# Optimization experiments

Hardware: AMD Instinct MI355X
Metric: run time of the kernel (lower is better)

Reference implementation:

```python
import jax, jax.numpy as jnp
import numpy as np

D_MODEL = 2048
NHEADS = 16
HEAD_DIM = D_MODEL // NHEADS


def setup_inputs() -> dict:
    key = jax.random.key(0)
    kx, kq, kk, kv, ko = jax.random.split(key, 5)
    B, S = 2, 2048
    scale = 1.0 / np.sqrt(D_MODEL)
    return {
        "x": jax.random.normal(kx, (B, S, D_MODEL), dtype=jnp.float32),
        "Wq": jax.random.normal(kq, (D_MODEL, D_MODEL), dtype=jnp.float32) * scale,
        "Wk": jax.random.normal(kk, (D_MODEL, D_MODEL), dtype=jnp.float32) * scale,
        "Wv": jax.random.normal(kv, (D_MODEL, D_MODEL), dtype=jnp.float32) * scale,
        "Wo": jax.random.normal(ko, (D_MODEL, D_MODEL), dtype=jnp.float32) * scale,
    }


def reference(x, Wq, Wk, Wv, Wo):
    B, S, _ = x.shape
    # nn.Linear(bias=False): y = x @ W.T
    q = (x @ Wq.T).reshape(B, S, NHEADS, HEAD_DIM)
    k = (x @ Wk.T).reshape(B, S, NHEADS, HEAD_DIM)
    v = (x @ Wv.T).reshape(B, S, NHEADS, HEAD_DIM)
    sm_scale = 1.0 / np.sqrt(HEAD_DIM)
    # scores: [B, H, S, S]
    scores = jnp.einsum("bqhd,bkhd->bhqk", q, k) * sm_scale
    causal_mask = jnp.tril(jnp.ones((S, S), dtype=bool))  # [S, S]
    scores = jnp.where(causal_mask, scores, jnp.finfo(scores.dtype).min)
    probs = jax.nn.softmax(scores, axis=-1)
    attn = jnp.einsum("bhqk,bkhd->bqhd", probs, v)  # [B, S, H, D]
    out = attn.reshape(B, S, D_MODEL) @ Wo.T
    return out
```

## Files before the change

kernel.cpp:

```cpp
#include <hip/hip_runtime.h>
#include <hip/hip_bf16.h>
#include <type_traits>

#define DEV __device__ __forceinline__

typedef __bf16 bf16x8 __attribute__((ext_vector_type(8)));
typedef float f32x4 __attribute__((ext_vector_type(4)));
typedef float f32x16 __attribute__((ext_vector_type(16)));
typedef unsigned short u16;
typedef unsigned int u32;

DEV u16 f32_to_bf16(float f) {
  union { float f; u32 u; } x; x.f = f;
  u32 r = (x.u + 0x7FFFu + ((x.u >> 16) & 1u)) >> 16;
  return (u16)r;
}

DEV u32 pack2(float a, float b) {
  union { __hip_bfloat162 h; u32 u; } c;
  c.h = __float22bfloat162_rn(float2{a, b});
  return c.u;
}

DEV void ld_lds16(const void* g, void* l) {
  __builtin_amdgcn_global_load_lds(
      (const __attribute__((address_space(1))) u32*)g,
      (__attribute__((address_space(3))) u32*)l, 16, 0, 0);
}

#define MFMA16(a, b, c) __builtin_amdgcn_mfma_f32_16x16x32_bf16(a, b, c, 0, 0, 0)
#define MFMA32(a, b, c) __builtin_amdgcn_mfma_f32_32x32x16_bf16(a, b, c, 0, 0, 0)

__global__ __launch_bounds__(256) void cast_all(
    const float* __restrict__ x,  const float* __restrict__ wq,
    const float* __restrict__ wk, const float* __restrict__ wv,
    const float* __restrict__ wo,
    u16* __restrict__ xb,  u16* __restrict__ wqb, u16* __restrict__ wkb,
    u16* __restrict__ wvb, u16* __restrict__ wob) {
  int bid = blockIdx.x;
  const float* src; u16* dst; int base;
  if (bid < 8192)       { src = x;  dst = xb;  base = bid; }
  else if (bid < 12288) { src = wq; dst = wqb; base = bid - 8192; }
  else if (bid < 16384) { src = wk; dst = wkb; base = bid - 12288; }
  else if (bid < 20480) { src = wv; dst = wvb; base = bid - 16384; }
  else                  { src = wo; dst = wob; base = bid - 20480; }
  int i = (base * 256 + threadIdx.x) * 4;
  float4 v = *reinterpret_cast<const float4*>(src + i);
  ushort4 o;
  o.x = f32_to_bf16(v.x); o.y = f32_to_bf16(v.y);
  o.z = f32_to_bf16(v.z); o.w = f32_to_bf16(v.w);
  *reinterpret_cast<ushort4*>(dst + i) = o;
}

template <typename OutT>
__global__ __launch_bounds__(256) void gemm_nt(const u16* __restrict__ A,
                                               const u16* __restrict__ B,
                                               OutT* __restrict__ C,
                                               int M, int N, int K,
                                               float oscLo, float oscHi, int nsplit) {
  __shared__ __align__(16) u16 sA[128 * 64];
  __shared__ __align__(16) u16 sB[128 * 64];
  const int tid = threadIdx.x;
  const int lane = tid & 63, wid = tid >> 6;
  const int lo = lane & 15, hi = lane >> 4;
  const int wm = wid >> 1, wn = wid & 1;
  const int m0 = blockIdx.y * 128, n0 = blockIdx.x * 128;
  const float osc = (n0 < nsplit) ? oscLo : oscHi;

  f32x4 acc[4][4] = {};

  for (int k0 = 0; k0 < K; k0 += 64) {
    __syncthreads();
#pragma unroll
    for (int i = 0; i < 4; ++i) {
      int e16 = i * 256 + tid;
      int r = e16 >> 3;
      int bcol = ((e16 & 7) * 16) ^ ((r & 7) << 4);
      int col = bcol >> 1;
      ld_lds16(A + (size_t)(m0 + r) * K + k0 + col, sA + e16 * 8);
      ld_lds16(B + (size_t)(n0 + r) * K + k0 + col, sB + e16 * 8);
    }
    __syncthreads();
#pragma unroll
    for (int kc = 0; kc < 2; ++kc) {
      bf16x8 a[4], b[4];
#pragma unroll
      for (int i = 0; i < 4; ++i) {
        int row = wm * 64 + i * 16 + lo;
        int boff = ((kc * 32 + hi * 8) * 2) ^ ((row & 7) << 4);
        a[i] = *(const bf16x8*)((const char*)sA + row * 128 + boff);
      }
#pragma unroll
      for (int i = 0; i < 4; ++i) {
        int row = wn * 64 + i * 16 + lo;
        int boff = ((kc * 32 + hi * 8) * 2) ^ ((row & 7) << 4);
        b[i] = *(const bf16x8*)((const char*)sB + row * 128 + boff);
      }
#pragma unroll
      for (int mi = 0; mi < 4; ++mi)
#pragma unroll
        for (int ni = 0; ni < 4; ++ni)
          acc[mi][ni] = MFMA16(a[mi], b[ni], acc[mi][ni]);
    }
  }
#pragma unroll
  for (int mi = 0; mi < 4; ++mi)
#pragma unroll
    for (int r = 0; r < 4; ++r) {
      size_t row = m0 + wm * 64 + mi * 16 + hi * 4 + r;
#pragma unroll
      for (int ni = 0; ni < 4; ++ni) {
        int col = n0 + wn * 64 + ni * 16 + lo;
        float v = acc[mi][ni][r] * osc;
        if constexpr (std::is_same<OutT, float>::value)
          C[row * N + col] = v;
        else
          C[row * N + col] = f32_to_bf16(v);
      }
    }
}

constexpr float RTHR2 = 11.5416f;

__global__ __launch_bounds__(256, 2) void attn_fwd(const u16* __restrict__ QK,
                                                   const u16* __restrict__ VT,
                                                   u16* __restrict__ O) {
  __shared__ __align__(16) u16 sK[2][64 * 128];

  const int x = blockIdx.x, h = blockIdx.y, b = blockIdx.z;
  const int qt = b ? x : (15 - x);
  const int tid = threadIdx.x;
  const int lane = tid & 63, wid = tid >> 6;
  const int l31 = lane & 31, hi5 = lane >> 5;

  const size_t baseQ = ((size_t)b * 2048) * 4096 + (size_t)h * 128;
  const size_t baseK = baseQ + 2048;
  const size_t baseV = ((size_t)h * 128) * 4096 + (size_t)b * 2048;
  const int q0 = qt * 128;
  const int qw = q0 + wid * 32;
  const int qg = qw + l31;
  const int nt = 2 * qt + 2;

  bf16x8 qf[8];
#pragma unroll
  for (int kc = 0; kc < 8; ++kc)
    qf[kc] = *(const bf16x8*)(QK + baseQ + (size_t)qg * 4096 + kc * 16 + hi5 * 8);

  f32x16 o[4] = {};
  float m = -INFINITY, ls = 0.f;

  auto stage = [&](int buf, int t) {
    const int kv = t * 64;
#pragma unroll
    for (int i = 0; i < 4; ++i) {
      int e = i * 256 + tid;
      int r = e >> 4;
      int bc = ((e & 15) * 16) ^ ((r & 7) << 4);
      ld_lds16(QK + baseK + (size_t)(kv + r) * 4096 + (bc >> 1), &sK[buf][e * 8]);
    }
  };

  stage(0, 0);

  for (int t = 0; t < nt; ++t) {
    __syncthreads();
    if (t + 1 < nt) stage((t + 1) & 1, t + 1);
    const int kv0 = t * 64;
    if (kv0 > qw + 31) continue;
    const u16* bK = sK[t & 1];

    f32x16 s[2] = {};
#pragma unroll
    for (int kb = 0; kb < 2; ++kb) {
      int row = kb * 32 + l31;
      int rsw = (row & 7) << 4;
#pragma unroll
      for (int kc = 0; kc < 8; ++kc) {
        int bo = (kc * 32 + hi5 * 16) ^ rsw;
        bf16x8 kf = *(const bf16x8*)((const char*)bK + row * 256 + bo);
        s[kb] = MFMA32(kf, qf[kc], s[kb]);
      }
    }

    bf16x8 vfr[4][4];
#pragma unroll
    for (int d = 0; d < 4; ++d)
#pragma unroll
      for (int ks = 0; ks < 4; ++ks)
        vfr[d][ks] = *(const bf16x8*)(VT + baseV + (size_t)(d * 32 + l31) * 4096 +
                                      kv0 + ks * 16 + hi5 * 8);

    if (kv0 + 63 > qw) {
#pragma unroll
      for (int kb = 0; kb < 2; ++kb)
#pragma unroll
        for (int j = 0; j < 16; ++j) {
          int keyg = kv0 + kb * 32 + (j & 3) + 8 * (j >> 2) + 4 * hi5;
          s[kb][j] = (keyg > qg) ? -3e38f : s[kb][j];
        }
    }

    float pmax = -3e38f;
#pragma unroll
    for (int kb = 0; kb < 2; ++kb)
#pragma unroll
      for (int j = 0; j < 16; ++j) pmax = fmaxf(pmax, s[kb][j]);
    pmax = fmaxf(pmax, __shfl_xor(pmax, 32));

    if (!__all(pmax - m <= RTHR2)) {
      float mn = fmaxf(m, pmax);
      float fr = exp2f(m - mn);
      ls *= fr;
#pragma unroll
      for (int d = 0; d < 4; ++d) o[d] *= fr;
      m = mn;
    }

    float rs = 0.f;
#pragma unroll
    for (int kb = 0; kb < 2; ++kb)
#pragma unroll
      for (int j = 0; j < 16; ++j) {
        float pv = exp2f(s[kb][j] - m);
        s[kb][j] = pv;
        rs += pv;
      }
    rs += __shfl_xor(rs, 32);
    ls += rs;

    union PF { u32 w[4]; bf16x8 v; };
    PF pf[4];
#pragma unroll
    for (int kb = 0; kb < 2; ++kb)
#pragma unroll
      for (int gp = 0; gp < 2; ++gp) {
        u32 keep[2], send[2];
#pragma unroll
        for (int w = 0; w < 2; ++w) {
          int ja = 8 * gp + 2 * w;
          int jb = 8 * gp + 4 + 2 * w;
          u32 aa = pack2(s[kb][ja], s[kb][ja + 1]);
          u32 bb = pack2(s[kb][jb], s[kb][jb + 1]);
          keep[w] = hi5 ? bb : aa;
          send[w] = hi5 ? aa : bb;
        }
        u32 recv0 = (u32)__shfl_xor((int)send[0], 32);
        u32 recv1 = (u32)__shfl_xor((int)send[1], 32);
        PF& f = pf[2 * kb + gp];
        f.w[0] = hi5 ? recv0 : keep[0];
        f.w[1] = hi5 ? recv1 : keep[1];
        f.w[2] = hi5 ? keep[0] : recv0;
        f.w[3] = hi5 ? keep[1] : recv1;
      }

#pragma unroll
    for (int d = 0; d < 4; ++d)
#pragma unroll
      for (int ks = 0; ks < 4; ++ks)
        o[d] = MFMA32(vfr[d][ks], pf[ks].v, o[d]);
  }

  float inv = 1.f / ls;
  size_t orow = (size_t)b * 2048 + qg;
#pragma unroll
  for (int d = 0; d < 4; ++d)
#pragma unroll
    for (int G = 0; G < 4; ++G) {
      union { u32 u[2]; ushort4 s4; } st;
      st.u[0] = pack2(o[d][4 * G + 0] * inv, o[d][4 * G + 1] * inv);
      st.u[1] = pack2(o[d][4 * G + 2] * inv, o[d][4 * G + 3] * inv);
      int col = h * 128 + d * 32 + 8 * G + 4 * hi5;
      *(ushort4*)(O + orow * 2048 + col) = st.s4;
    }
}

extern "C" void kernel_launch(void* const* d_in, const int* in_sizes, int n_in,
                              void* d_out, int out_size, void* d_ws, size_t ws_size,
                              hipStream_t stream) {
  const float* x  = (const float*)d_in[0];
  const float* Wq = (const float*)d_in[1];
  const float* Wk = (const float*)d_in[2];
  const float* Wv = (const float*)d_in[3];
  const float* Wo = (const float*)d_in[4];
  float* out = (float*)d_out;

  constexpr int B = 2, S = 2048, D = 2048;
  constexpr int M = B * S;
  constexpr float QSC = 0.12751742f;

  char* ws = (char*)d_ws;
  u16* xb  = (u16*)ws; ws += (size_t)M * D * 2;
  u16* wqb = (u16*)ws; ws += (size_t)D * D * 2;
  u16* wkb = (u16*)ws; ws += (size_t)D * D * 2;
  u16* wvb = (u16*)ws; ws += (size_t)D * D * 2;
  u16* wob = (u16*)ws; ws += (size_t)D * D * 2;
  u16* qk  = (u16*)ws; ws += (size_t)M * 2 * D * 2;
  u16* vT  = (u16*)ws; ws += (size_t)M * D * 2;
  u16* att = (u16*)ws; ws += (size_t)M * D * 2;

  cast_all<<<24576, 256, 0, stream>>>(x, Wq, Wk, Wv, Wo, xb, wqb, wkb, wvb, wob);

  gemm_nt<u16><<<dim3(32, 32), 256, 0, stream>>>(xb, wqb, qk, M, 2 * D, D,
                                                 QSC, 1.0f, D);
  gemm_nt<u16><<<dim3(M / 128, D / 128), 256, 0, stream>>>(wvb, xb, vT, D, M, D,
                                                           1.0f, 1.0f, 1 << 30);

  attn_fwd<<<dim3(16, 16, B), 256, 0, stream>>>(qk, vT, att);

  gemm_nt<float><<<dim3(D / 128, M / 128), 256, 0, stream>>>(att, wob, out, M, D, D,
                                                             1.0f, 1.0f, 1 << 30);
}
```

Measured before the change: 285.6 us.

## Add 256x256 double-buffered QK GEMM and stage V tiles through LDS in attention

Introduces a new 512-thread GEMM kernel with 256x256 tiles, double-buffered LDS, 32x32 MFMA, setprio hints and a block-index swizzle, and uses it for the fused Q/K projection. The attention kernel now loads V tiles into swizzled LDS alongside K instead of reading V fragments directly from global memory. The aim is more data reuse per tile and coalesced, overlapped V loads, in exchange for more LDS per block (128 KB in the GEMM), which may limit occupancy.

```diff
diff --git a/kernel.cpp b/kernel.cpp
--- a/kernel.cpp
+++ b/kernel.cpp
@@ -53,6 +53,103 @@
 }
 
 template <typename OutT>
+__global__ __launch_bounds__(512, 2) void gemm_nt256(
+    const u16* __restrict__ A, const u16* __restrict__ B, OutT* __restrict__ C,
+    int M, int N, int K, float oscLo, float oscHi, int nsplit, int nbx) {
+  __shared__ __align__(16) u16 sA[2][256 * 64];
+  __shared__ __align__(16) u16 sB[2][256 * 64];
+  const int tid = threadIdx.x;
+  const int lane = tid & 63, wid = tid >> 6;
+  const int l31 = lane & 31, hi5 = lane >> 5;
+  const int wm = wid >> 2, wn = wid & 3;
+  const int cpx = gridDim.x >> 3;
+  const int swz = ((int)blockIdx.x & 7) * cpx + ((int)blockIdx.x >> 3);
+  const int m0 = (swz / nbx) * 256, n0 = (swz % nbx) * 256;
+  const int NT = K >> 6;
+
+  f32x16 acc[4][2] = {};
+
+  auto stage = [&](int buf, int t) {
+    const int k0 = t << 6;
+#pragma unroll
+    for (int i = 0; i < 4; ++i) {
+      int e = i * 512 + tid;
+      int r = e >> 3;
+      int bc = ((e & 7) * 16) ^ ((r & 7) << 4);
+      ld_lds16(A + (size_t)(m0 + r) * K + k0 + (bc >> 1), &sA[buf][e * 8]);
+    }
+#pragma unroll
+    for (int i = 0; i < 4; ++i) {
+      int e = i * 512 + tid;
+      int r = e >> 3;
+      int bc = ((e & 7) * 16) ^ ((r & 7) << 4);
+      ld_lds16(B + (size_t)(n0 + r) * K + k0 + (bc >> 1), &sB[buf][e * 8]);
+    }
+  };
+
+  stage(0, 0);
+  __syncthreads();
+
+  for (int t = 0; t < NT; ++t) {
+    const u16* cA = sA[t & 1];
+    const u16* cB = sB[t & 1];
+    if (t + 1 < NT) stage((t + 1) & 1, t + 1);
+
+#pragma unroll
+    for (int kh = 0; kh < 2; ++kh) {
+      bf16x8 afr[4][2], bfr[2][2];
+#pragma unroll
+      for (int mi = 0; mi < 4; ++mi)
+#pragma unroll
+        for (int kc = 0; kc < 2; ++kc) {
+          int row = wm * 128 + mi * 32 + l31;
+          int bo = (((kh * 2 + kc) * 32 + hi5 * 16)) ^ ((row & 7) << 4);
+          afr[mi][kc] = *(const bf16x8*)((const char*)cA + row * 128 + bo);
+        }
+#pragma unroll
+      for (int ni = 0; ni < 2; ++ni)
+#pragma unroll
+        for (int kc = 0; kc < 2; ++kc) {
+          int row = wn * 64 + ni * 32 + l31;
+          int bo = (((kh * 2 + kc) * 32 + hi5 * 16)) ^ ((row & 7) << 4);
+          bfr[ni][kc] = *(const bf16x8*)((const char*)cB + row * 128 + bo);
+        }
+      asm volatile("s_waitcnt lgkmcnt(0)" ::: "memory");
+      __builtin_amdgcn_sched_barrier(0);
+      __builtin_amdgcn_s_setprio(1);
+#pragma unroll
+      for (int mi = 0; mi < 4; ++mi)
+#pragma unroll
+        for (int ni = 0; ni < 2; ++ni)
+#pragma unroll
+          for (int kc = 0; kc < 2; ++kc)
+            acc[mi][ni] = MFMA32(afr[mi][kc], bfr[ni][kc], acc[mi][ni]);
+      __builtin_amdgcn_s_setprio(0);
+      __builtin_amdgcn_sched_barrier(0);
+    }
+    __syncthreads();
+  }
+
+#pragma unroll
+  for (int mi = 0; mi < 4; ++mi)
+#pragma unroll
+    for (int ni = 0; ni < 2; ++ni) {
+      int colb = n0 + wn * 64 + ni * 32;
+      float osc = (colb < nsplit) ? oscLo : oscHi;
+      int col = colb + l31;
+#pragma unroll
+      for (int j = 0; j < 16; ++j) {
+        size_t row = m0 + wm * 128 + mi * 32 + (j & 3) + 8 * (j >> 2) + 4 * hi5;
+        float v = acc[mi][ni][j] * osc;
+        if constexpr (std::is_same<OutT, float>::value)
+          C[row * N + col] = v;
+        else
+          C[row * N + col] = f32_to_bf16(v);
+      }
+    }
+}
+
+template <typename OutT>
 __global__ __launch_bounds__(256) void gemm_nt(const u16* __restrict__ A,
                                                const u16* __restrict__ B,
                                                OutT* __restrict__ C,
@@ -126,6 +223,7 @@
                                                    const u16* __restrict__ VT,
                                                    u16* __restrict__ O) {
   __shared__ __align__(16) u16 sK[2][64 * 128];
+  __shared__ __align__(16) u16 sV[2][128 * 64];
 
   const int x = blockIdx.x, h = blockIdx.y, b = blockIdx.z;
   const int qt = b ? x : (15 - x);
@@ -158,6 +256,13 @@
       int bc = ((e & 15) * 16) ^ ((r & 7) << 4);
       ld_lds16(QK + baseK + (size_t)(kv + r) * 4096 + (bc >> 1), &sK[buf][e * 8]);
     }
+#pragma unroll
+    for (int i = 0; i < 4; ++i) {
+      int e = i * 256 + tid;
+      int r = e >> 3;
+      int bc = ((e & 7) * 16) ^ ((r & 7) << 4);
+      ld_lds16(VT + baseV + (size_t)r * 4096 + kv + (bc >> 1), &sV[buf][e * 8]);
+    }
   };
 
   stage(0, 0);
@@ -168,6 +273,7 @@
     const int kv0 = t * 64;
     if (kv0 > qw + 31) continue;
     const u16* bK = sK[t & 1];
+    const u16* bV = sV[t & 1];
 
     f32x16 s[2] = {};
 #pragma unroll
@@ -181,14 +287,6 @@
         s[kb] = MFMA32(kf, qf[kc], s[kb]);
       }
     }
-
-    bf16x8 vfr[4][4];
-#pragma unroll
-    for (int d = 0; d < 4; ++d)
-#pragma unroll
-      for (int ks = 0; ks < 4; ++ks)
-        vfr[d][ks] = *(const bf16x8*)(VT + baseV + (size_t)(d * 32 + l31) * 4096 +
-                                      kv0 + ks * 16 + hi5 * 8);
 
     if (kv0 + 63 > qw) {
 #pragma unroll
@@ -254,10 +352,16 @@
       }
 
 #pragma unroll
-    for (int d = 0; d < 4; ++d)
-#pragma unroll
-      for (int ks = 0; ks < 4; ++ks)
-        o[d] = MFMA32(vfr[d][ks], pf[ks].v, o[d]);
+    for (int d = 0; d < 4; ++d) {
+      int row = d * 32 + l31;
+      int rsw = (row & 7) << 4;
+#pragma unroll
+      for (int ks = 0; ks < 4; ++ks) {
+        int bo = (ks * 32 + hi5 * 16) ^ rsw;
+        bf16x8 vf = *(const bf16x8*)((const char*)bV + row * 128 + bo);
+        o[d] = MFMA32(vf, pf[ks].v, o[d]);
+      }
+    }
   }
 
   float inv = 1.f / ls;
@@ -300,8 +404,8 @@
 
   cast_all<<<24576, 256, 0, stream>>>(x, Wq, Wk, Wv, Wo, xb, wqb, wkb, wvb, wob);
 
-  gemm_nt<u16><<<dim3(32, 32), 256, 0, stream>>>(xb, wqb, qk, M, 2 * D, D,
-                                                 QSC, 1.0f, D);
+  gemm_nt256<u16><<<256, 512, 0, stream>>>(xb, wqb, qk, M, 2 * D, D,
+                                           QSC, 1.0f, D, 16);
   gemm_nt<u16><<<dim3(M / 128, D / 128), 256, 0, stream>>>(wvb, xb, vT, D, M, D,
                                                            1.0f, 1.0f, 1 << 30);
 
```

Result: faster. 261.4 us (-8.5%).

## Stage V tiles through LDS in attention and split QK output buffers

Applied to the files above, without the earlier changes.

The attention kernel now copies V^T tiles into double-buffered shared memory together with K, instead of each wave reading V fragments straight from global memory. The fused QK projection writes Q and K into separate contiguous buffers with row stride 2048, and the K swizzle is widened to 16 rows to match. s_setprio hints are placed around the MFMA blocks. LDS use per block doubles, which may limit occupancy under the 2-blocks-per-CU launch bound.

```diff
diff --git a/kernel.cpp b/kernel.cpp
--- a/kernel.cpp
+++ b/kernel.cpp
@@ -56,7 +56,8 @@
 __global__ __launch_bounds__(256) void gemm_nt(const u16* __restrict__ A,
                                                const u16* __restrict__ B,
                                                OutT* __restrict__ C,
-                                               int M, int N, int K,
+                                               OutT* __restrict__ C2,
+                                               int M, int N, int K, int ldc,
                                                float oscLo, float oscHi, int nsplit) {
   __shared__ __align__(16) u16 sA[128 * 64];
   __shared__ __align__(16) u16 sB[128 * 64];
@@ -65,7 +66,6 @@
   const int lo = lane & 15, hi = lane >> 4;
   const int wm = wid >> 1, wn = wid & 1;
   const int m0 = blockIdx.y * 128, n0 = blockIdx.x * 128;
-  const float osc = (n0 < nsplit) ? oscLo : oscHi;
 
   f32x4 acc[4][4] = {};
 
@@ -104,28 +104,34 @@
     }
   }
 #pragma unroll
-  for (int mi = 0; mi < 4; ++mi)
-#pragma unroll
-    for (int r = 0; r < 4; ++r) {
-      size_t row = m0 + wm * 64 + mi * 16 + hi * 4 + r;
-#pragma unroll
-      for (int ni = 0; ni < 4; ++ni) {
-        int col = n0 + wn * 64 + ni * 16 + lo;
+  for (int ni = 0; ni < 4; ++ni) {
+    int colb = n0 + wn * 64 + ni * 16;
+    bool lo_side = (colb < nsplit);
+    OutT* dst = lo_side ? C : C2;
+    float osc = lo_side ? oscLo : oscHi;
+    int col = (lo_side ? colb : colb - nsplit) + lo;
+#pragma unroll
+    for (int mi = 0; mi < 4; ++mi)
+#pragma unroll
+      for (int r = 0; r < 4; ++r) {
+        size_t row = m0 + wm * 64 + mi * 16 + hi * 4 + r;
         float v = acc[mi][ni][r] * osc;
         if constexpr (std::is_same<OutT, float>::value)
-          C[row * N + col] = v;
+          dst[row * ldc + col] = v;
         else
-          C[row * N + col] = f32_to_bf16(v);
-      }
-    }
+          dst[row * ldc + col] = f32_to_bf16(v);
+      }
+  }
 }
 
 constexpr float RTHR2 = 11.5416f;
 
-__global__ __launch_bounds__(256, 2) void attn_fwd(const u16* __restrict__ QK,
+__global__ __launch_bounds__(256, 2) void attn_fwd(const u16* __restrict__ Q,
+                                                   const u16* __restrict__ K,
                                                    const u16* __restrict__ VT,
                                                    u16* __restrict__ O) {
   __shared__ __align__(16) u16 sK[2][64 * 128];
+  __shared__ __align__(16) u16 sV[2][128 * 64];
 
   const int x = blockIdx.x, h = blockIdx.y, b = blockIdx.z;
   const int qt = b ? x : (15 - x);
@@ -133,9 +139,8 @@
   const int lane = tid & 63, wid = tid >> 6;
   const int l31 = lane & 31, hi5 = lane >> 5;
 
-  const size_t baseQ = ((size_t)b * 2048) * 4096 + (size_t)h * 128;
-  const size_t baseK = baseQ + 2048;
-  const size_t baseV = ((size_t)h * 128) * 4096 + (size_t)b * 2048;
+  const size_t baseQK = ((size_t)b * 2048) * 2048 + (size_t)h * 128;
+  const size_t baseV  = ((size_t)h * 128) * 4096 + (size_t)b * 2048;
   const int q0 = qt * 128;
   const int qw = q0 + wid * 32;
   const int qg = qw + l31;
@@ -144,7 +149,7 @@
   bf16x8 qf[8];
 #pragma unroll
   for (int kc = 0; kc < 8; ++kc)
-    qf[kc] = *(const bf16x8*)(QK + baseQ + (size_t)qg * 4096 + kc * 16 + hi5 * 8);
+    qf[kc] = *(const bf16x8*)(Q + baseQK + (size_t)qg * 2048 + kc * 16 + hi5 * 8);
 
   f32x16 o[4] = {};
   float m = -INFINITY, ls = 0.f;
@@ -155,8 +160,15 @@
     for (int i = 0; i < 4; ++i) {
       int e = i * 256 + tid;
       int r = e >> 4;
-      int bc = ((e & 15) * 16) ^ ((r & 7) << 4);
-      ld_lds16(QK + baseK + (size_t)(kv + r) * 4096 + (bc >> 1), &sK[buf][e * 8]);
+      int bc = ((e & 15) * 16) ^ ((r & 15) << 4);
+      ld_lds16(K + baseQK + (size_t)(kv + r) * 2048 + (bc >> 1), &sK[buf][e * 8]);
+    }
+#pragma unroll
+    for (int i = 0; i < 4; ++i) {
+      int e = i * 256 + tid;
+      int r = e >> 3;
+      int bc = ((e & 7) * 16) ^ ((r & 7) << 4);
+      ld_lds16(VT + baseV + (size_t)r * 4096 + kv + (bc >> 1), &sV[buf][e * 8]);
     }
   };
 
@@ -168,12 +180,14 @@
     const int kv0 = t * 64;
     if (kv0 > qw + 31) continue;
     const u16* bK = sK[t & 1];
+    const u16* bV = sV[t & 1];
 
     f32x16 s[2] = {};
+    __builtin_amdgcn_s_setprio(1);
 #pragma unroll
     for (int kb = 0; kb < 2; ++kb) {
       int row = kb * 32 + l31;
-      int rsw = (row & 7) << 4;
+      int rsw = (row & 15) << 4;
 #pragma unroll
       for (int kc = 0; kc < 8; ++kc) {
         int bo = (kc * 32 + hi5 * 16) ^ rsw;
@@ -181,14 +195,7 @@
         s[kb] = MFMA32(kf, qf[kc], s[kb]);
       }
     }
-
-    bf16x8 vfr[4][4];
-#pragma unroll
-    for (int d = 0; d < 4; ++d)
-#pragma unroll
-      for (int ks = 0; ks < 4; ++ks)
-        vfr[d][ks] = *(const bf16x8*)(VT + baseV + (size_t)(d * 32 + l31) * 4096 +
-                                      kv0 + ks * 16 + hi5 * 8);
+    __builtin_amdgcn_s_setprio(0);
 
     if (kv0 + 63 > qw) {
 #pragma unroll
@@ -253,11 +260,19 @@
         f.w[3] = hi5 ? keep[1] : recv1;
       }
 
-#pragma unroll
-    for (int d = 0; d < 4; ++d)
-#pragma unroll
-      for (int ks = 0; ks < 4; ++ks)
-        o[d] = MFMA32(vfr[d][ks], pf[ks].v, o[d]);
+    __builtin_amdgcn_s_setprio(1);
+#pragma unroll
+    for (int d = 0; d < 4; ++d) {
+      int row = d * 32 + l31;
+      int rsw = (row & 7) << 4;
+#pragma unroll
+      for (int ks = 0; ks < 4; ++ks) {
+        int bo = (ks * 32 + hi5 * 16) ^ rsw;
+        bf16x8 vf = *(const bf16x8*)((const char*)bV + row * 128 + bo);
+        o[d] = MFMA32(vf, pf[ks].v, o[d]);
+      }
+    }
+    __builtin_amdgcn_s_setprio(0);
   }
 
   float inv = 1.f / ls;
@@ -287,6 +302,7 @@
   constexpr int B = 2, S = 2048, D = 2048;
   constexpr int M = B * S;
   constexpr float QSC = 0.12751742f;
+  constexpr int NOSPLIT = 1 << 30;
 
   char* ws = (char*)d_ws;
   u16* xb  = (u16*)ws; ws += (size_t)M * D * 2;
@@ -294,19 +310,20 @@
   u16* wkb = (u16*)ws; ws += (size_t)D * D * 2;
   u16* wvb = (u16*)ws; ws += (size_t)D * D * 2;
   u16* wob = (u16*)ws; ws += (size_t)D * D * 2;
-  u16* qk  = (u16*)ws; ws += (size_t)M * 2 * D * 2;
+  u16* q   = (u16*)ws; ws += (size_t)M * D * 2;
+  u16* k   = (u16*)ws; ws += (size_t)M * D * 2;
   u16* vT  = (u16*)ws; ws += (size_t)M * D * 2;
   u16* att = (u16*)ws; ws += (size_t)M * D * 2;
 
   cast_all<<<24576, 256, 0, stream>>>(x, Wq, Wk, Wv, Wo, xb, wqb, wkb, wvb, wob);
 
-  gemm_nt<u16><<<dim3(32, 32), 256, 0, stream>>>(xb, wqb, qk, M, 2 * D, D,
+  gemm_nt<u16><<<dim3(32, 32), 256, 0, stream>>>(xb, wqb, q, k, M, 2 * D, D, D,
                                                  QSC, 1.0f, D);
-  gemm_nt<u16><<<dim3(M / 128, D / 128), 256, 0, stream>>>(wvb, xb, vT, D, M, D,
-                                                           1.0f, 1.0f, 1 << 30);
-
-  attn_fwd<<<dim3(16, 16, B), 256, 0, stream>>>(qk, vT, att);
-
-  gemm_nt<float><<<dim3(D / 128, M / 128), 256, 0, stream>>>(att, wob, out, M, D, D,
-                                                             1.0f, 1.0f, 1 << 30);
-}
+  gemm_nt<u16><<<dim3(32, 16), 256, 0, stream>>>(wvb, xb, vT, vT, D, M, D, M,
+                                                 1.0f, 1.0f, NOSPLIT);
+
+  attn_fwd<<<dim3(16, 16, B), 256, 0, stream>>>(q, k, vT, att);
+
+  gemm_nt<float><<<dim3(16, 32), 256, 0, stream>>>(att, wob, out, out, M, D, D, D,
+                                                   1.0f, 1.0f, NOSPLIT);
+}
```

Result: faster. 272.3 us (-4.6%).
